# Optimization experiments

Hardware: AMD Instinct MI355X
Metric: run time of the kernel (lower is better)

## Reference

```python
import jax, jax.numpy as jnp
import numpy as np

N_NODES = 50000
N_EDGES = 600000
IN_DIM = 128
OUT_DIM = 1024


def setup_inputs() -> dict:
    key = jax.random.key(0)
    k1, k2, k3 = jax.random.split(key, 3)
    x = jax.random.normal(k1, (N_NODES, IN_DIM), dtype=jnp.float32)
    edge_index = jax.random.randint(k2, (2, N_EDGES), 0, N_NODES, dtype=jnp.int64)
    # Linear(3*in_dim, out_dim): weight stored as [3*in_dim, out_dim] for x @ W
    W = jax.random.normal(k3, (3 * IN_DIM, OUT_DIM), dtype=jnp.float32) * (1.0 / np.sqrt(3 * IN_DIM))
    b = jnp.zeros((OUT_DIM,), dtype=jnp.float32)
    return {"x": x, "edge_index": edge_index, "W": W, "b": b}


def _mean_aggregate(feats, seg_ids, n):
    # segment-mean: sum gathered features per segment, divide by count (>=1)
    s = jax.ops.segment_sum(feats, seg_ids, num_segments=n)          # [N, d]
    cnt = jax.ops.segment_sum(jnp.ones((feats.shape[0],), feats.dtype), seg_ids, num_segments=n)
    return s / jnp.maximum(cnt, 1.0)[:, None]


def reference(x, edge_index, W, b):
    n = x.shape[0]
    src = edge_index[0]
    dst = edge_index[1]
    # mean over in-neighbors (messages flow src -> dst)
    mean_in = _mean_aggregate(x[src], dst, n)
    # mean over out-neighbors (messages flow dst -> src)
    mean_out = _mean_aggregate(x[dst], src, n)
    h = jnp.concatenate([x, mean_in, mean_out], axis=-1)             # [N, 3*in_dim]
    return jax.nn.relu(h @ W + b)                                    # [N, out_dim]
```

## Files before the change

kernel.cpp:

```cpp
#include <hip/hip_runtime.h>
#include <hip/hip_bf16.h>


typedef __attribute__((ext_vector_type(8))) short bf16x8;
typedef __attribute__((ext_vector_type(4))) short bf16x4;
typedef __attribute__((ext_vector_type(4))) float f32x4;

#define IN_DIM 128
#define K3 384
#define ODIM 1024

static __device__ inline short bfs(float f) {
    union { __hip_bfloat16 b; short s; } u;
    u.b = __float2bfloat16(f);
    return u.s;
}

__global__ __launch_bounds__(256) void sage_prep(
    const float* __restrict__ x, const int* __restrict__ src,
    const int* __restrict__ dst, const float* __restrict__ W,
    __hip_bfloat16* __restrict__ xb, __hip_bfloat16* __restrict__ h,
    __hip_bfloat16* __restrict__ Wt, int* __restrict__ deg,
    int n_nodes, int n_edges, int wtB, int convB)
{
    int b = blockIdx.x;
    int t = threadIdx.x;
    if (b < wtB) {
        __shared__ __hip_bfloat16 lds[32][36];
        int tk = b / 32, tn = b % 32;
        int k0 = tk * 32, n0 = tn * 32;
        int r = t >> 3, c = (t & 7) * 4;
        f32x4 w = *(const f32x4*)(W + (size_t)(k0 + r) * ODIM + n0 + c);
#pragma unroll
        for (int i = 0; i < 4; ++i) lds[c + i][r] = __float2bfloat16(w[i]);
        __syncthreads();
        *(bf16x4*)&Wt[(size_t)(n0 + r) * K3 + k0 + c] = *(bf16x4*)&lds[r][c];
        return;
    }
    b -= wtB;
    if (b < convB) {
        int tid = b * 256 + t;
        if (tid >= n_nodes * 16) return;
        int i = tid >> 4, d8 = (tid & 15) << 3;
        const float* xp = x + (size_t)i * IN_DIM + d8;
        f32x4 a = *(const f32x4*)xp;
        f32x4 c4 = *(const f32x4*)(xp + 4);
        bf16x8 v;
        v[0] = bfs(a.x); v[1] = bfs(a.y); v[2] = bfs(a.z); v[3] = bfs(a.w);
        v[4] = bfs(c4.x); v[5] = bfs(c4.y); v[6] = bfs(c4.z); v[7] = bfs(c4.w);
        *(bf16x8*)(xb + (size_t)i * IN_DIM + d8) = v;
        *(bf16x8*)(h + (size_t)i * K3 + d8) = v;
        return;
    }
    b -= convB;
    int e = b * 256 + t;
    if (e >= n_edges) return;
    atomicAdd(deg + dst[e], 1);
    atomicAdd(deg + n_nodes + src[e], 1);
}

__global__ __launch_bounds__(256) void scan_partial(
    const int* __restrict__ deg, int* __restrict__ off, int* __restrict__ bsum, int n)
{
    __shared__ int s[256];
    int t = threadIdx.x;
    int base = blockIdx.x * 1024 + t * 4;
    int4 v = {0, 0, 0, 0};
    if (base + 3 < n) v = *(const int4*)(deg + base);
    else {
        if (base     < n) v.x = deg[base];
        if (base + 1 < n) v.y = deg[base + 1];
        if (base + 2 < n) v.z = deg[base + 2];
        if (base + 3 < n) v.w = deg[base + 3];
    }
    int tsum = v.x + v.y + v.z + v.w;
    s[t] = tsum;
    __syncthreads();
#pragma unroll
    for (int d = 1; d < 256; d <<= 1) {
        int add = (t >= d) ? s[t - d] : 0;
        __syncthreads();
        s[t] += add;
        __syncthreads();
    }
    int excl = s[t] - tsum;
    if (t == 255) bsum[blockIdx.x] = s[255];
    int e0 = excl, e1 = e0 + v.x, e2 = e1 + v.y, e3 = e2 + v.z;
    if (base     < n) off[base]     = e0;
    if (base + 1 < n) off[base + 1] = e1;
    if (base + 2 < n) off[base + 2] = e2;
    if (base + 3 < n) off[base + 3] = e3;
}

__global__ __launch_bounds__(256) void scan_bsum(int* __restrict__ bsum, int nblk)
{
    __shared__ int s[256];
    int t = threadIdx.x;
    int v = (t < nblk) ? bsum[t] : 0;
    s[t] = v;
    __syncthreads();
#pragma unroll
    for (int d = 1; d < 256; d <<= 1) {
        int add = (t >= d) ? s[t - d] : 0;
        __syncthreads();
        s[t] += add;
        __syncthreads();
    }
    if (t < nblk) bsum[t] = s[t] - v;
}

__global__ __launch_bounds__(256) void scan_add(
    int* __restrict__ off, int* __restrict__ cursor,
    const int* __restrict__ bsum, int n)
{
    int base = blockIdx.x * 1024 + threadIdx.x * 4;
    int b = bsum[blockIdx.x];
#pragma unroll
    for (int j = 0; j < 4; ++j)
        if (base + j < n) {
            int v = off[base + j] + b;
            off[base + j]    = v;
            cursor[base + j] = v;
        }
}

__global__ __launch_bounds__(256) void sage_fill(
    const int* __restrict__ src, const int* __restrict__ dst,
    int* __restrict__ cursor, int* __restrict__ csr, int n_nodes, int n_edges)
{
    int t = blockIdx.x * 256 + threadIdx.x;
    if (t >= n_edges) return;
    int s = src[t];
    int d = dst[t];
    int p0 = atomicAdd(cursor + d, 1);
    csr[p0] = s;
    int p1 = atomicAdd(cursor + n_nodes + s, 1);
    csr[p1] = d;
}

__global__ __launch_bounds__(256) void sage_aggregate(
    const __hip_bfloat16* __restrict__ xb, const int* __restrict__ csr,
    const int* __restrict__ off, const int* __restrict__ deg,
    __hip_bfloat16* __restrict__ h, int n_nodes)
{
    int wid  = (int)((blockIdx.x * 256 + threadIdx.x) >> 6);
    int lane = threadIdx.x & 63;
    if (wid >= 2 * n_nodes) return;
    int i = wid >> 1;
    int d = wid & 1;
    int idx = i + d * n_nodes;

    float2 a = {0.f, 0.f};
    int b0 = off[idx], dg = deg[idx];

#define GATHER(nb) { \
    __hip_bfloat162 v = ((const __hip_bfloat162*)(xb + (size_t)(nb) * IN_DIM))[lane]; \
    a.x += __low2float(v); a.y += __high2float(v); }

    int e = 0;
    for (; e + 3 < dg; e += 4) {
        int a0 = csr[b0 + e], a1 = csr[b0 + e + 1], a2 = csr[b0 + e + 2], a3 = csr[b0 + e + 3];
        GATHER(a0) GATHER(a1) GATHER(a2) GATHER(a3)
    }
    for (; e < dg; ++e) { int a0 = csr[b0 + e]; GATHER(a0) }
#undef GATHER

    float inv = 1.0f / (float)max(dg, 1);
    __hip_bfloat162 p;
    p.x = __float2bfloat16(a.x * inv);
    p.y = __float2bfloat16(a.y * inv);
    ((__hip_bfloat162*)(h + (size_t)i * K3))[64 + (d << 6) + lane] = p;
}

__global__ __launch_bounds__(256, 4) void sage_gemm(
    const __hip_bfloat16* __restrict__ h, const __hip_bfloat16* __restrict__ Wt,
    const float* __restrict__ bias, float* __restrict__ out, int n_nodes)
{
    __shared__ __hip_bfloat16 Asm[2][128 * 32];
    __shared__ __hip_bfloat16 Bsm[2][128 * 32];

    int t    = threadIdx.x;
    int wave = t >> 6;
    int lane = t & 63;

    int bid = blockIdx.x;
    int sid = bid;
    if ((gridDim.x & 7) == 0) {
        int cpx = gridDim.x >> 3;
        sid = (bid & 7) * cpx + (bid >> 3);
    }
    int tn   = sid & 7;
    int tm   = sid >> 3;
    int m0   = tm * 128;
    int n0   = tn * 128;
    int wm   = wave >> 1;
    int wn   = wave & 1;
    int m    = lane & 15;
    int quad = lane >> 4;

    int srow = t >> 2;
    int seg  = t & 3;
    int g    = seg ^ (srow & 3);
    int ga0  = m0 + srow;       if (ga0 >= n_nodes) ga0 = n_nodes - 1;
    int ga1  = m0 + srow + 64;  if (ga1 >= n_nodes) ga1 = n_nodes - 1;
    const __hip_bfloat16* gA0 = h  + (size_t)ga0 * K3 + g * 8;
    const __hip_bfloat16* gA1 = h  + (size_t)ga1 * K3 + g * 8;
    const __hip_bfloat16* gB0 = Wt + (size_t)(n0 + srow) * K3 + g * 8;
    const __hip_bfloat16* gB1 = Wt + (size_t)(n0 + srow + 64) * K3 + g * 8;
    int l0 = (0 * 256 + wave * 64) * 8;
    int l1 = (1 * 256 + wave * 64) * 8;

    f32x4 acc[4][4];
#pragma unroll
    for (int s = 0; s < 4; ++s)
#pragma unroll
        for (int u = 0; u < 4; ++u) acc[s][u] = (f32x4){0.f, 0.f, 0.f, 0.f};

    __builtin_amdgcn_global_load_lds(gA0, &Asm[0][l0], 16, 0, 0);
    __builtin_amdgcn_global_load_lds(gA1, &Asm[0][l1], 16, 0, 0);
    __builtin_amdgcn_global_load_lds(gB0, &Bsm[0][l0], 16, 0, 0);
    __builtin_amdgcn_global_load_lds(gB1, &Bsm[0][l1], 16, 0, 0);

    int slot = quad ^ (m & 3);
#pragma unroll
    for (int kt = 0; kt < 12; ++kt) {
        int p = kt & 1;
        __syncthreads();
        if (kt < 11) {
            int koff = (kt + 1) * 32;
            __builtin_amdgcn_global_load_lds(gA0 + koff, &Asm[p ^ 1][l0], 16, 0, 0);
            __builtin_amdgcn_global_load_lds(gA1 + koff, &Asm[p ^ 1][l1], 16, 0, 0);
            __builtin_amdgcn_global_load_lds(gB0 + koff, &Bsm[p ^ 1][l0], 16, 0, 0);
            __builtin_amdgcn_global_load_lds(gB1 + koff, &Bsm[p ^ 1][l1], 16, 0, 0);
        }
        bf16x8 a[4], b[4];
#pragma unroll
        for (int s = 0; s < 4; ++s) {
            int row = wm * 64 + s * 16 + m;
            a[s] = *(const bf16x8*)&Asm[p][row * 32 + slot * 8];
        }
#pragma unroll
        for (int u = 0; u < 4; ++u) {
            int row = wn * 64 + u * 16 + m;
            b[u] = *(const bf16x8*)&Bsm[p][row * 32 + slot * 8];
        }
#pragma unroll
        for (int s = 0; s < 4; ++s)
#pragma unroll
            for (int u = 0; u < 4; ++u)
                acc[s][u] = __builtin_amdgcn_mfma_f32_16x16x32_bf16(a[s], b[u], acc[s][u], 0, 0, 0);
    }

    float bv[4];
#pragma unroll
    for (int u = 0; u < 4; ++u) bv[u] = bias[n0 + wn * 64 + u * 16 + m];

    bool full = (m0 + 128 <= n_nodes);
    if (full) {
#pragma unroll
        for (int s = 0; s < 4; ++s) {
            int r0 = m0 + wm * 64 + s * 16 + quad * 4;
#pragma unroll
            for (int r = 0; r < 4; ++r) {
                float* orow = out + (size_t)(r0 + r) * ODIM + n0 + wn * 64 + m;
#pragma unroll
                for (int u = 0; u < 4; ++u)
                    __builtin_nontemporal_store(fmaxf(acc[s][u][r] + bv[u], 0.f), orow + u * 16);
            }
        }
    } else {
#pragma unroll
        for (int s = 0; s < 4; ++s) {
            int r0 = m0 + wm * 64 + s * 16 + quad * 4;
#pragma unroll
            for (int r = 0; r < 4; ++r) {
                if (r0 + r >= n_nodes) continue;
                float* orow = out + (size_t)(r0 + r) * ODIM + n0 + wn * 64 + m;
#pragma unroll
                for (int u = 0; u < 4; ++u)
                    __builtin_nontemporal_store(fmaxf(acc[s][u][r] + bv[u], 0.f), orow + u * 16);
            }
        }
    }
}

extern "C" void kernel_launch(void* const* d_in, const int* in_sizes, int n_in,
                              void* d_out, int out_size, void* d_ws, size_t ws_size,
                              hipStream_t stream)
{
    const float* x    = (const float*)d_in[0];
    const int*   ei   = (const int*)d_in[1];
    const float* W    = (const float*)d_in[2];
    const float* bias = (const float*)d_in[3];

    int n_nodes = in_sizes[0] / IN_DIM;
    int n_edges = in_sizes[1] / 2;
    const int* src = ei;
    const int* dst = ei + n_edges;
    int n2 = 2 * n_nodes;

    char* ws = (char*)d_ws;
    int* deg    = (int*)ws;
    int* cursor = deg + n2;
    int* off    = cursor + n2;
    int* bsum   = off + n2;
    int* csr    = bsum + 256;
    __hip_bfloat16* h  = (__hip_bfloat16*)(csr + 2 * n_edges);
    __hip_bfloat16* Wt = h  + (size_t)n_nodes * K3;
    __hip_bfloat16* xb = Wt + (size_t)K3 * ODIM;

    hipMemsetAsync(deg, 0, (size_t)n2 * sizeof(int), stream);

    int wtB   = (K3 / 32) * (ODIM / 32);
    int convB = (n_nodes * 16 + 255) / 256;
    int degB  = (n_edges + 255) / 256;
    sage_prep<<<wtB + convB + degB, 256, 0, stream>>>(
        x, src, dst, W, xb, h, Wt, deg, n_nodes, n_edges, wtB, convB);

    int nblk = (n2 + 1023) / 1024;
    scan_partial<<<nblk, 256, 0, stream>>>(deg, off, bsum, n2);
    scan_bsum<<<1, 256, 0, stream>>>(bsum, nblk);
    scan_add<<<nblk, 256, 0, stream>>>(off, cursor, bsum, n2);

    sage_fill<<<degB, 256, 0, stream>>>(src, dst, cursor, csr, n_nodes, n_edges);

    sage_aggregate<<<(n2 + 3) / 4, 256, 0, stream>>>(xb, csr, off, deg, h, n_nodes);

    int tiles_m = (n_nodes + 127) / 128;
    int blocks  = tiles_m * (ODIM / 128);
    sage_gemm<<<blocks, 256, 0, stream>>>(h, Wt, bias, (float*)d_out, n_nodes);
}
```

Before: 462.8 us.

## Split concatenated h buffer, read x directly in GEMM, one thread per edge-direction

Drops the duplicate write of the bf16 copy of x into the concatenated h buffer. The GEMM now streams its first 128 K columns from xb and the remaining 256 from a separate aggregate buffer. The degree-count and CSR-fill kernels use one thread per edge direction, doubling the grid but issuing one atomic per thread. The aggregation loop is unrolled to 8 neighbors to keep more gathers in flight. These changes cut redundant global writes and raise memory-level parallelism, at the cost of a per-iteration pointer select inside the GEMM K loop.

Result: no change. 465.1 us (+0.5%).

```diff
diff --git a/kernel.cpp b/kernel.cpp
--- a/kernel.cpp
+++ b/kernel.cpp
@@ -7,6 +7,7 @@
 typedef __attribute__((ext_vector_type(4))) float f32x4;
 
 #define IN_DIM 128
+#define AGG 256
 #define K3 384
 #define ODIM 1024
 
@@ -19,9 +20,8 @@
 __global__ __launch_bounds__(256) void sage_prep(
     const float* __restrict__ x, const int* __restrict__ src,
     const int* __restrict__ dst, const float* __restrict__ W,
-    __hip_bfloat16* __restrict__ xb, __hip_bfloat16* __restrict__ h,
-    __hip_bfloat16* __restrict__ Wt, int* __restrict__ deg,
-    int n_nodes, int n_edges, int wtB, int convB)
+    __hip_bfloat16* __restrict__ xb, __hip_bfloat16* __restrict__ Wt,
+    int* __restrict__ deg, int n_nodes, int n_edges, int wtB, int convB)
 {
     int b = blockIdx.x;
     int t = threadIdx.x;
@@ -49,14 +49,13 @@
         v[0] = bfs(a.x); v[1] = bfs(a.y); v[2] = bfs(a.z); v[3] = bfs(a.w);
         v[4] = bfs(c4.x); v[5] = bfs(c4.y); v[6] = bfs(c4.z); v[7] = bfs(c4.w);
         *(bf16x8*)(xb + (size_t)i * IN_DIM + d8) = v;
-        *(bf16x8*)(h + (size_t)i * K3 + d8) = v;
         return;
     }
     b -= convB;
     int e = b * 256 + t;
-    if (e >= n_edges) return;
-    atomicAdd(deg + dst[e], 1);
-    atomicAdd(deg + n_nodes + src[e], 1);
+    if (e >= 2 * n_edges) return;
+    int idx = (e < n_edges) ? dst[e] : n_nodes + src[e - n_edges];
+    atomicAdd(deg + idx, 1);
 }
 
 __global__ __launch_bounds__(256) void scan_partial(
@@ -129,19 +128,18 @@
     int* __restrict__ cursor, int* __restrict__ csr, int n_nodes, int n_edges)
 {
     int t = blockIdx.x * 256 + threadIdx.x;
-    if (t >= n_edges) return;
-    int s = src[t];
-    int d = dst[t];
-    int p0 = atomicAdd(cursor + d, 1);
-    csr[p0] = s;
-    int p1 = atomicAdd(cursor + n_nodes + s, 1);
-    csr[p1] = d;
+    if (t >= 2 * n_edges) return;
+    int node, val;
+    if (t < n_edges) { node = dst[t]; val = src[t]; }
+    else { int e = t - n_edges; node = n_nodes + src[e]; val = dst[e]; }
+    int p = atomicAdd(cursor + node, 1);
+    csr[p] = val;
 }
 
 __global__ __launch_bounds__(256) void sage_aggregate(
     const __hip_bfloat16* __restrict__ xb, const int* __restrict__ csr,
     const int* __restrict__ off, const int* __restrict__ deg,
-    __hip_bfloat16* __restrict__ h, int n_nodes)
+    __hip_bfloat16* __restrict__ hagg, int n_nodes)
 {
     int wid  = (int)((blockIdx.x * 256 + threadIdx.x) >> 6);
     int lane = threadIdx.x & 63;
@@ -152,29 +150,37 @@
 
     float2 a = {0.f, 0.f};
     int b0 = off[idx], dg = deg[idx];
+    const int* cp = csr + b0;
 
 #define GATHER(nb) { \
     __hip_bfloat162 v = ((const __hip_bfloat162*)(xb + (size_t)(nb) * IN_DIM))[lane]; \
     a.x += __low2float(v); a.y += __high2float(v); }
 
     int e = 0;
+    for (; e + 7 < dg; e += 8) {
+        int a0 = cp[e],     a1 = cp[e + 1], a2 = cp[e + 2], a3 = cp[e + 3];
+        int a4 = cp[e + 4], a5 = cp[e + 5], a6 = cp[e + 6], a7 = cp[e + 7];
+        GATHER(a0) GATHER(a1) GATHER(a2) GATHER(a3)
+        GATHER(a4) GATHER(a5) GATHER(a6) GATHER(a7)
+    }
     for (; e + 3 < dg; e += 4) {
-        int a0 = csr[b0 + e], a1 = csr[b0 + e + 1], a2 = csr[b0 + e + 2], a3 = csr[b0 + e + 3];
+        int a0 = cp[e], a1 = cp[e + 1], a2 = cp[e + 2], a3 = cp[e + 3];
         GATHER(a0) GATHER(a1) GATHER(a2) GATHER(a3)
     }
-    for (; e < dg; ++e) { int a0 = csr[b0 + e]; GATHER(a0) }
+    for (; e < dg; ++e) { int a0 = cp[e]; GATHER(a0) }
 #undef GATHER
 
     float inv = 1.0f / (float)max(dg, 1);
     __hip_bfloat162 p;
     p.x = __float2bfloat16(a.x * inv);
     p.y = __float2bfloat16(a.y * inv);
-    ((__hip_bfloat162*)(h + (size_t)i * K3))[64 + (d << 6) + lane] = p;
+    ((__hip_bfloat162*)(hagg + (size_t)i * AGG))[(d << 6) + lane] = p;
 }
 
 __global__ __launch_bounds__(256, 4) void sage_gemm(
-    const __hip_bfloat16* __restrict__ h, const __hip_bfloat16* __restrict__ Wt,
-    const float* __restrict__ bias, float* __restrict__ out, int n_nodes)
+    const __hip_bfloat16* __restrict__ xb, const __hip_bfloat16* __restrict__ hagg,
+    const __hip_bfloat16* __restrict__ Wt, const float* __restrict__ bias,
+    float* __restrict__ out, int n_nodes)
 {
     __shared__ __hip_bfloat16 Asm[2][128 * 32];
     __shared__ __hip_bfloat16 Bsm[2][128 * 32];
@@ -203,8 +209,10 @@
     int g    = seg ^ (srow & 3);
     int ga0  = m0 + srow;       if (ga0 >= n_nodes) ga0 = n_nodes - 1;
     int ga1  = m0 + srow + 64;  if (ga1 >= n_nodes) ga1 = n_nodes - 1;
-    const __hip_bfloat16* gA0 = h  + (size_t)ga0 * K3 + g * 8;
-    const __hip_bfloat16* gA1 = h  + (size_t)ga1 * K3 + g * 8;
+    const __hip_bfloat16* xA0 = xb   + (size_t)ga0 * IN_DIM + g * 8;
+    const __hip_bfloat16* xA1 = xb   + (size_t)ga1 * IN_DIM + g * 8;
+    const __hip_bfloat16* hA0 = hagg + (size_t)ga0 * AGG    + g * 8;
+    const __hip_bfloat16* hA1 = hagg + (size_t)ga1 * AGG    + g * 8;
     const __hip_bfloat16* gB0 = Wt + (size_t)(n0 + srow) * K3 + g * 8;
     const __hip_bfloat16* gB1 = Wt + (size_t)(n0 + srow + 64) * K3 + g * 8;
     int l0 = (0 * 256 + wave * 64) * 8;
@@ -216,8 +224,8 @@
 #pragma unroll
         for (int u = 0; u < 4; ++u) acc[s][u] = (f32x4){0.f, 0.f, 0.f, 0.f};
 
-    __builtin_amdgcn_global_load_lds(gA0, &Asm[0][l0], 16, 0, 0);
-    __builtin_amdgcn_global_load_lds(gA1, &Asm[0][l1], 16, 0, 0);
+    __builtin_amdgcn_global_load_lds(xA0, &Asm[0][l0], 16, 0, 0);
+    __builtin_amdgcn_global_load_lds(xA1, &Asm[0][l1], 16, 0, 0);
     __builtin_amdgcn_global_load_lds(gB0, &Bsm[0][l0], 16, 0, 0);
     __builtin_amdgcn_global_load_lds(gB1, &Bsm[0][l1], 16, 0, 0);
 
@@ -227,11 +235,13 @@
         int p = kt & 1;
         __syncthreads();
         if (kt < 11) {
-            int koff = (kt + 1) * 32;
-            __builtin_amdgcn_global_load_lds(gA0 + koff, &Asm[p ^ 1][l0], 16, 0, 0);
-            __builtin_amdgcn_global_load_lds(gA1 + koff, &Asm[p ^ 1][l1], 16, 0, 0);
-            __builtin_amdgcn_global_load_lds(gB0 + koff, &Bsm[p ^ 1][l0], 16, 0, 0);
-            __builtin_amdgcn_global_load_lds(gB1 + koff, &Bsm[p ^ 1][l1], 16, 0, 0);
+            int kn = kt + 1;
+            const __hip_bfloat16* pA0 = (kn < 4) ? xA0 + kn * 32 : hA0 + (kn - 4) * 32;
+            const __hip_bfloat16* pA1 = (kn < 4) ? xA1 + kn * 32 : hA1 + (kn - 4) * 32;
+            __builtin_amdgcn_global_load_lds(pA0, &Asm[p ^ 1][l0], 16, 0, 0);
+            __builtin_amdgcn_global_load_lds(pA1, &Asm[p ^ 1][l1], 16, 0, 0);
+            __builtin_amdgcn_global_load_lds(gB0 + kn * 32, &Bsm[p ^ 1][l0], 16, 0, 0);
+            __builtin_amdgcn_global_load_lds(gB1 + kn * 32, &Bsm[p ^ 1][l1], 16, 0, 0);
         }
         bf16x8 a[4], b[4];
 #pragma unroll
@@ -305,17 +315,17 @@
     int* off    = cursor + n2;
     int* bsum   = off + n2;
     int* csr    = bsum + 256;
-    __hip_bfloat16* h  = (__hip_bfloat16*)(csr + 2 * n_edges);
-    __hip_bfloat16* Wt = h  + (size_t)n_nodes * K3;
-    __hip_bfloat16* xb = Wt + (size_t)K3 * ODIM;
+    __hip_bfloat16* hagg = (__hip_bfloat16*)(csr + 2 * n_edges);
+    __hip_bfloat16* Wt   = hagg + (size_t)n_nodes * AGG;
+    __hip_bfloat16* xb   = Wt + (size_t)K3 * ODIM;
 
     hipMemsetAsync(deg, 0, (size_t)n2 * sizeof(int), stream);
 
     int wtB   = (K3 / 32) * (ODIM / 32);
     int convB = (n_nodes * 16 + 255) / 256;
-    int degB  = (n_edges + 255) / 256;
+    int degB  = (2 * n_edges + 255) / 256;
     sage_prep<<<wtB + convB + degB, 256, 0, stream>>>(
-        x, src, dst, W, xb, h, Wt, deg, n_nodes, n_edges, wtB, convB);
+        x, src, dst, W, xb, Wt, deg, n_nodes, n_edges, wtB, convB);
 
     int nblk = (n2 + 1023) / 1024;
     scan_partial<<<nblk, 256, 0, stream>>>(deg, off, bsum, n2);
@@ -324,9 +334,9 @@
 
     sage_fill<<<degB, 256, 0, stream>>>(src, dst, cursor, csr, n_nodes, n_edges);
 
-    sage_aggregate<<<(n2 + 3) / 4, 256, 0, stream>>>(xb, csr, off, deg, h, n_nodes);
+    sage_aggregate<<<(n2 + 3) / 4, 256, 0, stream>>>(xb, csr, off, deg, hagg, n_nodes);
 
     int tiles_m = (n_nodes + 127) / 128;
     int blocks  = tiles_m * (ODIM / 128);
-    sage_gemm<<<blocks, 256, 0, stream>>>(h, Wt, bias, (float*)d_out, n_nodes);
-}
+    sage_gemm<<<blocks, 256, 0, stream>>>(xb, hagg, Wt, bias, (float*)d_out, n_nodes);
+}
```
